# Kernel optimization log

Hardware: AMD Instinct MI355X
Metric: run time of the kernel (lower is better)

## Reference

```python
import jax, jax.numpy as jnp
import numpy as np

N_DRUG = 20000
N_DIS = 20000
D = 128
E = 640000
L = 200000


def _sage(x_src, x_dst, src, dst, Wl, Wr, b, n_dst):
    # SAGEConv: out_i = lin_l(mean_{j in N(i)} x_src_j) + lin_r(x_dst_i)
    msg = x_src[src]                                   # [E, D] gather
    agg = jax.ops.segment_sum(msg, dst, num_segments=n_dst)
    cnt = jax.ops.segment_sum(jnp.ones((src.shape[0],), x_src.dtype), dst,
                              num_segments=n_dst)
    mean = agg / jnp.maximum(cnt, 1.0)[:, None]
    return mean @ Wl + b + x_dst @ Wr


def setup_inputs() -> dict:
    key = jax.random.key(0)
    ks = jax.random.split(key, 24)
    s = 1.0 / np.sqrt(D)
    inp = {
        "x_drug": jax.random.normal(ks[0], (N_DRUG, D), jnp.float32),
        "x_disease": jax.random.normal(ks[1], (N_DIS, D), jnp.float32),
        "ei_d2s": jax.random.randint(ks[2], (2, E), 0, 20000),
        "ei_s2d": jax.random.randint(ks[3], (2, E), 0, 20000),
        "edge_label_index": jax.random.randint(ks[4], (2, L), 0, 20000),
    }
    names = ["W1l_d2s", "W1r_d2s", "W1l_s2d", "W1r_s2d",
             "W2l_d2s", "W2r_d2s", "W2l_s2d", "W2r_s2d"]
    for i, n in enumerate(names):
        inp[n] = jax.random.uniform(ks[5 + i], (D, D), jnp.float32, -s, s)
    for i, n in enumerate(["b1_d2s", "b1_s2d", "b2_d2s", "b2_s2d"]):
        inp[n] = jax.random.uniform(ks[13 + i], (D,), jnp.float32, -s, s)
    inp["dec_W1"] = jax.random.uniform(ks[17], (2 * D, D), jnp.float32, -s, s)
    inp["dec_b1"] = jax.random.uniform(ks[18], (D,), jnp.float32, -s, s)
    inp["dec_W2"] = jax.random.uniform(ks[19], (D, 1), jnp.float32, -s, s)
    inp["dec_b2"] = jax.random.uniform(ks[20], (1,), jnp.float32, -s, s)
    return inp


def reference(x_drug, x_disease,
              W1l_d2s, W1r_d2s, b1_d2s, W1l_s2d, W1r_s2d, b1_s2d,
              W2l_d2s, W2r_d2s, b2_d2s, W2l_s2d, W2r_s2d, b2_s2d,
              dec_W1, dec_b1, dec_W2, dec_b2,
              ei_d2s, ei_s2d, edge_label_index):
    # --- hetero GNN encoder, layer 1 (relu) ---
    h_dis = jax.nn.relu(_sage(x_drug, x_disease, ei_d2s[0], ei_d2s[1],
                              W1l_d2s, W1r_d2s, b1_d2s, N_DIS))
    h_drug = jax.nn.relu(_sage(x_disease, x_drug, ei_s2d[0], ei_s2d[1],
                               W1l_s2d, W1r_s2d, b1_s2d, N_DRUG))
    # --- layer 2 (no activation) ---
    z_dis = _sage(h_drug, h_dis, ei_d2s[0], ei_d2s[1],
                  W2l_d2s, W2r_d2s, b2_d2s, N_DIS)
    z_drug = _sage(h_dis, h_drug, ei_s2d[0], ei_s2d[1],
                   W2l_s2d, W2r_s2d, b2_s2d, N_DRUG)
    # --- edge decoder: gather, concat, 2-layer MLP ---
    row, col = edge_label_index[0], edge_label_index[1]
    z = jnp.concatenate([z_drug[row], z_dis[col]], axis=-1)   # [L, 2D]
    z = jax.nn.relu(z @ dec_W1 + dec_b1)
    z = z @ dec_W2 + dec_b2
    return z.reshape(-1)
```

## Files before the change

### kernel.cpp

```cpp
#include <hip/hip_runtime.h>
#include <hip/hip_fp16.h>

#define D 128
#define NDRUG 20000
#define NDIS 20000
#define EDGES 640000
#define LROWS 200000
#define ROWP 264

typedef unsigned short u16;
typedef __attribute__((ext_vector_type(8))) _Float16 h8v;
typedef __attribute__((ext_vector_type(4))) float f4v;


__device__ inline void h8_load(uint4 u, float f[8]) {
    float2 a = __half22float2(*(const __half2*)&u.x);
    float2 b = __half22float2(*(const __half2*)&u.y);
    float2 c = __half22float2(*(const __half2*)&u.z);
    float2 d = __half22float2(*(const __half2*)&u.w);
    f[0] = a.x; f[1] = a.y; f[2] = b.x; f[3] = b.y;
    f[4] = c.x; f[5] = c.y; f[6] = d.x; f[7] = d.y;
}

__global__ __launch_bounds__(256) void rank2_kernel(
    const int* __restrict__ dA, int* __restrict__ cA, int* __restrict__ rA,
    const int* __restrict__ dB, int* __restrict__ cB, int* __restrict__ rB, int n)
{
    int i = blockIdx.x * blockDim.x + threadIdx.x;
    if (i < n) rA[i] = atomicAdd(&cA[dA[i]], 1);
    else if (i - n < n) rB[i - n] = atomicAdd(&cB[dB[i - n]], 1);
}

__global__ __launch_bounds__(1024) void scan2_kernel(int* __restrict__ c0, int* __restrict__ o0,
                                                     int* __restrict__ c1, int* __restrict__ o1,
                                                     int n) {
    int* cnt_io = (blockIdx.x == 0) ? c0 : c1;
    int* off    = (blockIdx.x == 0) ? o0 : o1;
    __shared__ int wsum[16];
    __shared__ int carry_s;
    const int tid = threadIdx.x;
    const int lane = tid & 63;
    const int wid = tid >> 6;
    if (tid == 0) { carry_s = 0; off[0] = 0; }
    __syncthreads();
    for (int start = 0; start < n; start += 1024) {
        int i = start + tid;
        int v = (i < n) ? cnt_io[i] : 0;
        int carry = carry_s;
        int s = v;
        #pragma unroll
        for (int o = 1; o < 64; o <<= 1) {
            int t = __shfl_up(s, o, 64);
            if (lane >= o) s += t;
        }
        if (lane == 63) wsum[wid] = s;
        __syncthreads();
        if (wid == 0) {
            int ws = (lane < 16) ? wsum[lane] : 0;
            #pragma unroll
            for (int o = 1; o < 16; o <<= 1) {
                int t = __shfl_up(ws, o, 64);
                if (lane >= o) ws += t;
            }
            if (lane < 16) wsum[lane] = ws;
        }
        __syncthreads();
        int woff = (wid > 0) ? wsum[wid - 1] : 0;
        int incl = s + woff + carry;
        if (i < n) {
            off[i + 1] = incl;
            cnt_io[i] = incl - v;
        }
        __syncthreads();
        if (tid == 1023) carry_s = incl;
        __syncthreads();
    }
}

#define SB 104

__global__ __launch_bounds__(256) void scatter_sliced_kernel(
    const int* __restrict__ srcA, const int* __restrict__ dstA,
    const int* __restrict__ rkA, const int* __restrict__ offA, u16* __restrict__ csrA,
    const int* __restrict__ srcB, const int* __restrict__ dstB,
    const int* __restrict__ rkB, const int* __restrict__ offB, u16* __restrict__ csrB,
    int n)
{
    int b = blockIdx.x;
    int dirB = (b >= 8 * SB);
    int bb = b - (dirB ? 8 * SB : 0);
    int s = bb & 7;
    int sub = bb >> 3;
    const int* src = dirB ? srcB : srcA;
    const int* dst = dirB ? dstB : dstA;
    const int* rk  = dirB ? rkB : rkA;
    const int* off = dirB ? offB : offA;
    u16* csr = dirB ? csrB : csrA;

    const int lo = s * 2500, hi = lo + 2500;
    const int chunk = (n + SB - 1) / SB;
    int i0 = sub * chunk;
    int i1 = i0 + chunk; i1 = i1 < n ? i1 : n;
    for (int i = i0 + threadIdx.x; i < i1; i += 256) {
        int d = dst[i];
        if (d >= lo && d < hi) {
            int pos = off[d] + rk[i];
            csr[pos] = (u16)src[i];
        }
    }
}


__global__ __launch_bounds__(256) void cvt16_kernel(const float* __restrict__ in,
                                                    __half* __restrict__ out, int n4) {
    int i = blockIdx.x * blockDim.x + threadIdx.x;
    if (i >= n4) return;
    float4 v = ((const float4*)in)[i];
    __half2 a = __floats2half2_rn(v.x, v.y);
    __half2 b = __floats2half2_rn(v.z, v.w);
    uint2 u;
    u.x = *(unsigned*)&a;
    u.y = *(unsigned*)&b;
    ((uint2*)out)[i] = u;
}

__global__ __launch_bounds__(256) void cvtwt_kernel(
    const float* __restrict__ W1l_d2s, const float* __restrict__ W1r_d2s,
    const float* __restrict__ W1l_s2d, const float* __restrict__ W1r_s2d,
    const float* __restrict__ W2l_d2s, const float* __restrict__ W2r_d2s,
    const float* __restrict__ W2l_s2d, const float* __restrict__ W2r_s2d,
    const float* __restrict__ decW1, __half* __restrict__ out)
{
    int gid = blockIdx.x * 256 + threadIdx.x;
    float v;
    if (gid < 4 * 32768) {
        int chunk = gid >> 15;
        int r = gid & 32767;
        int col = r >> 8;
        int k = r & 255;
        const float *Wl, *Wr;
        switch (chunk) {
            case 0: Wl = W1l_d2s; Wr = W1r_d2s; break;
            case 1: Wl = W1l_s2d; Wr = W1r_s2d; break;
            case 2: Wl = W2l_d2s; Wr = W2r_d2s; break;
            default: Wl = W2l_s2d; Wr = W2r_s2d; break;
        }
        const float* src = (k < 128) ? Wl : Wr;
        v = src[(size_t)(k & 127) * D + col];
    } else {
        int r = gid - 4 * 32768;
        int chunk = r >> 14;
        int q = r & 16383;
        int col = q >> 7;
        int k = q & 127;
        int row = k + (chunk == 0 ? 128 : 0);
        v = decW1[(size_t)row * D + col];
    }
    out[gid] = __float2half_rn(v);
}


__device__ inline void sage_gather(
    const __half* __restrict__ xsrc, const __half* __restrict__ xdst,
    const int* __restrict__ off, const u16* __restrict__ csr,
    __half sm[16][ROWP], int node0, int row0, int lane)
{
    const bool hiHalf = lane >= 32;
    const int lq = lane & 31;
    const int c0 = lq * 4;
    for (int r = 0; r < 4; ++r) {
        int node = node0 + r;
        int e0 = off[node], e1 = off[node + 1];
        int deg = e1 - e0;
        float a0 = 0.f, a1 = 0.f, a2 = 0.f, a3 = 0.f;
        for (int base = e0; base < e1; base += 64) {
            int nv = e1 - base; nv = nv < 64 ? nv : 64;
            int myidx = 0;
            if (lane < nv) myidx = csr[base + lane];
            int npair = nv >> 1;
            int t = 0;
            for (; t + 4 <= npair; t += 4) {
                int pa0 = __builtin_amdgcn_readlane(myidx, 2 * t + 0);
                int pb0 = __builtin_amdgcn_readlane(myidx, 2 * t + 1);
                int pa1 = __builtin_amdgcn_readlane(myidx, 2 * t + 2);
                int pb1 = __builtin_amdgcn_readlane(myidx, 2 * t + 3);
                int pa2 = __builtin_amdgcn_readlane(myidx, 2 * t + 4);
                int pb2 = __builtin_amdgcn_readlane(myidx, 2 * t + 5);
                int pa3 = __builtin_amdgcn_readlane(myidx, 2 * t + 6);
                int pb3 = __builtin_amdgcn_readlane(myidx, 2 * t + 7);
                int s0 = hiHalf ? pb0 : pa0;
                int s1 = hiHalf ? pb1 : pa1;
                int s2 = hiHalf ? pb2 : pa2;
                int s3 = hiHalf ? pb3 : pa3;
                uint2 u0 = *(const uint2*)(xsrc + (size_t)s0 * D + c0);
                uint2 u1 = *(const uint2*)(xsrc + (size_t)s1 * D + c0);
                uint2 u2 = *(const uint2*)(xsrc + (size_t)s2 * D + c0);
                uint2 u3 = *(const uint2*)(xsrc + (size_t)s3 * D + c0);
                float2 t0, t1;
                t0 = __half22float2(*(const __half2*)&u0.x);
                t1 = __half22float2(*(const __half2*)&u0.y);
                a0 += t0.x; a1 += t0.y; a2 += t1.x; a3 += t1.y;
                t0 = __half22float2(*(const __half2*)&u1.x);
                t1 = __half22float2(*(const __half2*)&u1.y);
                a0 += t0.x; a1 += t0.y; a2 += t1.x; a3 += t1.y;
                t0 = __half22float2(*(const __half2*)&u2.x);
                t1 = __half22float2(*(const __half2*)&u2.y);
                a0 += t0.x; a1 += t0.y; a2 += t1.x; a3 += t1.y;
                t0 = __half22float2(*(const __half2*)&u3.x);
                t1 = __half22float2(*(const __half2*)&u3.y);
                a0 += t0.x; a1 += t0.y; a2 += t1.x; a3 += t1.y;
            }
            for (; t < npair; ++t) {
                int pa = __builtin_amdgcn_readlane(myidx, 2 * t + 0);
                int pb = __builtin_amdgcn_readlane(myidx, 2 * t + 1);
                int s = hiHalf ? pb : pa;
                uint2 u = *(const uint2*)(xsrc + (size_t)s * D + c0);
                float2 t0 = __half22float2(*(const __half2*)&u.x);
                float2 t1 = __half22float2(*(const __half2*)&u.y);
                a0 += t0.x; a1 += t0.y; a2 += t1.x; a3 += t1.y;
            }
            if (nv & 1) {
                int s = __builtin_amdgcn_readlane(myidx, nv - 1);
                if (!hiHalf) {
                    uint2 u = *(const uint2*)(xsrc + (size_t)s * D + c0);
                    float2 t0 = __half22float2(*(const __half2*)&u.x);
                    float2 t1 = __half22float2(*(const __half2*)&u.y);
                    a0 += t0.x; a1 += t0.y; a2 += t1.x; a3 += t1.y;
                }
            }
        }
        a0 += __shfl_xor(a0, 32, 64);
        a1 += __shfl_xor(a1, 32, 64);
        a2 += __shfl_xor(a2, 32, 64);
        a3 += __shfl_xor(a3, 32, 64);
        float inv = 1.0f / (float)(deg < 1 ? 1 : deg);
        if (!hiHalf) {
            __half2 h01 = __floats2half2_rn(a0 * inv, a1 * inv);
            __half2 h23 = __floats2half2_rn(a2 * inv, a3 * inv);
            uint2 w; w.x = *(unsigned*)&h01; w.y = *(unsigned*)&h23;
            *(uint2*)&sm[row0 + r][c0] = w;
        } else {
            uint2 u = *(const uint2*)(xdst + (size_t)node * D + c0);
            *(uint2*)&sm[row0 + r][128 + c0] = u;
        }
    }
}


__global__ __launch_bounds__(256, 4) void sage_l1_kernel(
    const __half* __restrict__ xsA, const __half* __restrict__ xdA,
    const int* __restrict__ offA, const u16* __restrict__ csrA,
    const __half* __restrict__ wTA, const float* __restrict__ bA, __half* __restrict__ outA,
    const __half* __restrict__ xsB, const __half* __restrict__ xdB,
    const int* __restrict__ offB, const u16* __restrict__ csrB,
    const __half* __restrict__ wTB, const float* __restrict__ bB, __half* __restrict__ outB)
{
    __shared__ __align__(16) __half sm[16][ROWP];
    const int s8 = blockIdx.x & 7;
    const int bank = s8 >> 2;
    const int blk = ((int)blockIdx.x >> 3) * 4 + (s8 & 3);
    if (blk >= NDIS / 16) return;
    const __half* xsrc = bank ? xsB : xsA;
    const __half* xdst = bank ? xdB : xdA;
    const int* off = bank ? offB : offA;
    const u16* csr = bank ? csrB : csrA;
    const __half* wT = bank ? wTB : wTA;
    const float* bias = bank ? bB : bA;
    __half* out16 = bank ? outB : outA;

    const int lane = threadIdx.x & 63;
    const int wid = threadIdx.x >> 6;
    const int node0 = blk * 16;

    sage_gather(xsrc, xdst, off, csr, sm, node0 + wid * 4, wid * 4, lane);
    __syncthreads();

    const int lr = lane & 15;
    const int g = lane >> 4;
    const int colbase = wid * 32;
    f4v acc0 = {0.f, 0.f, 0.f, 0.f};
    f4v acc1 = {0.f, 0.f, 0.f, 0.f};
    #pragma unroll
    for (int t = 0; t < 8; ++t) {
        h8v a = *(const h8v*)&sm[lr][t * 32 + g * 8];
        h8v b0 = *(const h8v*)(wT + (size_t)(colbase + lr) * 256 + t * 32 + g * 8);
        h8v b1 = *(const h8v*)(wT + (size_t)(colbase + 16 + lr) * 256 + t * 32 + g * 8);
        acc0 = __builtin_amdgcn_mfma_f32_16x16x32_f16(a, b0, acc0, 0, 0, 0);
        acc1 = __builtin_amdgcn_mfma_f32_16x16x32_f16(a, b1, acc1, 0, 0, 0);
    }
    #pragma unroll
    for (int reg = 0; reg < 4; ++reg) {
        int row = g * 4 + reg;
        int col0 = colbase + lr;
        int col1 = colbase + 16 + lr;
        float v0 = fmaxf(acc0[reg] + bias[col0], 0.f);
        float v1 = fmaxf(acc1[reg] + bias[col1], 0.f);
        out16[(size_t)(node0 + row) * D + col0] = __float2half_rn(v0);
        out16[(size_t)(node0 + row) * D + col1] = __float2half_rn(v1);
    }
}

__global__ __launch_bounds__(256, 4) void sage_l2_kernel(
    const __half* __restrict__ xsA, const __half* __restrict__ xdA,
    const int* __restrict__ offA, const u16* __restrict__ csrA,
    const __half* __restrict__ wTA, const float* __restrict__ bA,
    const __half* __restrict__ wdTA, const float* __restrict__ pbA, __half* __restrict__ PoutA,
    const __half* __restrict__ xsB, const __half* __restrict__ xdB,
    const int* __restrict__ offB, const u16* __restrict__ csrB,
    const __half* __restrict__ wTB, const float* __restrict__ bB,
    const __half* __restrict__ wdTB, const float* __restrict__ pbB, __half* __restrict__ PoutB)
{
    __shared__ __align__(16) __half sm[16][ROWP];
    const int s8 = blockIdx.x & 7;
    const int bank = s8 >> 2;
    const int blk = ((int)blockIdx.x >> 3) * 4 + (s8 & 3);
    if (blk >= NDIS / 16) return;
    const __half* xsrc = bank ? xsB : xsA;
    const __half* xdst = bank ? xdB : xdA;
    const int* off = bank ? offB : offA;
    const u16* csr = bank ? csrB : csrA;
    const __half* wT = bank ? wTB : wTA;
    const float* bias = bank ? bB : bA;
    const __half* wdT = bank ? wdTB : wdTA;
    const float* pb = bank ? pbB : pbA;
    __half* Pout = bank ? PoutB : PoutA;

    const int lane = threadIdx.x & 63;
    const int wid = threadIdx.x >> 6;
    const int node0 = blk * 16;

    sage_gather(xsrc, xdst, off, csr, sm, node0 + wid * 4, wid * 4, lane);
    __syncthreads();

    const int lr = lane & 15;
    const int g = lane >> 4;
    const int colbase = wid * 32;
    f4v acc0 = {0.f, 0.f, 0.f, 0.f};
    f4v acc1 = {0.f, 0.f, 0.f, 0.f};
    #pragma unroll
    for (int t = 0; t < 8; ++t) {
        h8v a = *(const h8v*)&sm[lr][t * 32 + g * 8];
        h8v b0 = *(const h8v*)(wT + (size_t)(colbase + lr) * 256 + t * 32 + g * 8);
        h8v b1 = *(const h8v*)(wT + (size_t)(colbase + 16 + lr) * 256 + t * 32 + g * 8);
        acc0 = __builtin_amdgcn_mfma_f32_16x16x32_f16(a, b0, acc0, 0, 0, 0);
        acc1 = __builtin_amdgcn_mfma_f32_16x16x32_f16(a, b1, acc1, 0, 0, 0);
    }

    __syncthreads();
    #pragma unroll
    for (int reg = 0; reg < 4; ++reg) {
        int row = g * 4 + reg;
        sm[row][colbase + lr] = __float2half_rn(acc0[reg] + bias[colbase + lr]);
        sm[row][colbase + 16 + lr] = __float2half_rn(acc1[reg] + bias[colbase + 16 + lr]);
    }
    __syncthreads();

    f4v p0 = {0.f, 0.f, 0.f, 0.f};
    f4v p1 = {0.f, 0.f, 0.f, 0.f};
    #pragma unroll
    for (int t = 0; t < 4; ++t) {
        h8v a = *(const h8v*)&sm[lr][t * 32 + g * 8];
        h8v b0 = *(const h8v*)(wdT + (size_t)(colbase + lr) * 128 + t * 32 + g * 8);
        h8v b1 = *(const h8v*)(wdT + (size_t)(colbase + 16 + lr) * 128 + t * 32 + g * 8);
        p0 = __builtin_amdgcn_mfma_f32_16x16x32_f16(a, b0, p0, 0, 0, 0);
        p1 = __builtin_amdgcn_mfma_f32_16x16x32_f16(a, b1, p1, 0, 0, 0);
    }
    #pragma unroll
    for (int reg = 0; reg < 4; ++reg) {
        int row = g * 4 + reg;
        int col0 = colbase + lr;
        int col1 = colbase + 16 + lr;
        float v0 = p0[reg] + (pb ? pb[col0] : 0.f);
        float v1 = p1[reg] + (pb ? pb[col1] : 0.f);
        Pout[(size_t)(node0 + row) * D + col0] = __float2half_rn(v0);
        Pout[(size_t)(node0 + row) * D + col1] = __float2half_rn(v1);
    }
}


__global__ __launch_bounds__(256) void dec_gather_kernel(
    const __half* __restrict__ Pd, const __half* __restrict__ Ps,
    const int* __restrict__ row_idx, const int* __restrict__ col_idx,
    const float* __restrict__ W2, const float* __restrict__ b2,
    float* __restrict__ out, int nrows)
{
    const int lane = threadIdx.x & 63;
    const int wid = threadIdx.x >> 6;
    const int g = lane >> 4;
    const int lq = lane & 15;
    const int wave_id = blockIdx.x * 4 + wid;
    const int e0 = wave_id * 32;
    if (e0 >= nrows) return;

    const int c0 = lq * 8;
    float w2v[8];
    #pragma unroll
    for (int i = 0; i < 8; ++i) w2v[i] = W2[c0 + i];
    float b2v = b2[0];

    #pragma unroll 2
    for (int it = 0; it < 8; ++it) {
        int ei = it * 4 + g;
        int rr = e0 + ei;
        int ri = row_idx[rr];
        int ci = col_idx[rr];
        uint4 ua = *(const uint4*)(Pd + (size_t)ri * D + c0);
        uint4 ub = *(const uint4*)(Ps + (size_t)ci * D + c0);
        float fa[8], fb[8];
        h8_load(ua, fa);
        h8_load(ub, fb);
        float v = 0.f;
        #pragma unroll
        for (int i = 0; i < 8; ++i)
            v = fmaf(fmaxf(fa[i] + fb[i], 0.f), w2v[i], v);
        v += __shfl_xor(v, 1, 64);
        v += __shfl_xor(v, 2, 64);
        v += __shfl_xor(v, 4, 64);
        v += __shfl_xor(v, 8, 64);
        if (lq == 0) out[rr] = v + b2v;
    }
}


extern "C" void kernel_launch(void* const* d_in, const int* in_sizes, int n_in,
                              void* d_out, int out_size, void* d_ws, size_t ws_size,
                              hipStream_t stream) {
    const float* x_drug = (const float*)d_in[0];
    const float* x_dis  = (const float*)d_in[1];
    const int* ei_d2s = (const int*)d_in[2];
    const int* ei_s2d = (const int*)d_in[3];
    const int* ell    = (const int*)d_in[4];
    const float* W1l_d2s = (const float*)d_in[5];
    const float* W1r_d2s = (const float*)d_in[6];
    const float* W1l_s2d = (const float*)d_in[7];
    const float* W1r_s2d = (const float*)d_in[8];
    const float* W2l_d2s = (const float*)d_in[9];
    const float* W2r_d2s = (const float*)d_in[10];
    const float* W2l_s2d = (const float*)d_in[11];
    const float* W2r_s2d = (const float*)d_in[12];
    const float* b1_d2s = (const float*)d_in[13];
    const float* b1_s2d = (const float*)d_in[14];
    const float* b2_d2s = (const float*)d_in[15];
    const float* b2_s2d = (const float*)d_in[16];
    const float* dec_W1 = (const float*)d_in[17];
    const float* dec_b1 = (const float*)d_in[18];
    const float* dec_W2 = (const float*)d_in[19];
    const float* dec_b2 = (const float*)d_in[20];
    float* out = (float*)d_out;

    char* ws = (char*)d_ws;
    size_t o = 0;
    auto take = [&](size_t bytes) -> char* {
        char* p = ws + o;
        o += (bytes + 255) & ~(size_t)255;
        return p;
    };
    int* off_d2s = (int*)take((NDIS + 1) * sizeof(int));
    int* cnt_d2s = (int*)take(NDIS * sizeof(int));
    u16* csr_d2s = (u16*)take((size_t)EDGES * sizeof(u16));
    int* rk_d2s  = (int*)take((size_t)EDGES * sizeof(int));
    int* off_s2d = (int*)take((NDRUG + 1) * sizeof(int));
    int* cnt_s2d = (int*)take(NDRUG * sizeof(int));
    u16* csr_s2d = (u16*)take((size_t)EDGES * sizeof(u16));
    int* rk_s2d  = (int*)take((size_t)EDGES * sizeof(int));
    __half* x16_drug = (__half*)take((size_t)NDRUG * D * sizeof(__half));
    __half* x16_dis  = (__half*)take((size_t)NDIS * D * sizeof(__half));
    __half* h16_dis  = (__half*)take((size_t)NDIS * D * sizeof(__half));
    __half* h16_drug = (__half*)take((size_t)NDRUG * D * sizeof(__half));
    __half* P16_drug = (__half*)take((size_t)NDRUG * D * sizeof(__half));
    __half* P16_dis  = (__half*)take((size_t)NDIS * D * sizeof(__half));
    __half* w16 = (__half*)take((size_t)163840 * sizeof(__half));

    __half* wT_l1_d2s = w16 + 0 * 32768;
    __half* wT_l1_s2d = w16 + 1 * 32768;
    __half* wT_l2_d2s = w16 + 2 * 32768;
    __half* wT_l2_s2d = w16 + 3 * 32768;
    __half* wdT_hi    = w16 + 4 * 32768;
    __half* wdT_lo    = w16 + 4 * 32768 + 16384;

    hipMemsetAsync(cnt_d2s, 0, NDIS * sizeof(int), stream);
    hipMemsetAsync(cnt_s2d, 0, NDRUG * sizeof(int), stream);

    cvtwt_kernel<<<640, 256, 0, stream>>>(
        W1l_d2s, W1r_d2s, W1l_s2d, W1r_s2d,
        W2l_d2s, W2r_d2s, W2l_s2d, W2r_s2d, dec_W1, w16);

    cvt16_kernel<<<(NDRUG * D / 4 + 255) / 256, 256, 0, stream>>>(x_drug, x16_drug, NDRUG * D / 4);
    cvt16_kernel<<<(NDIS * D / 4 + 255) / 256, 256, 0, stream>>>(x_dis, x16_dis, NDIS * D / 4);

    const int EB2 = (2 * EDGES + 255) / 256;
    rank2_kernel<<<EB2, 256, 0, stream>>>(ei_d2s + EDGES, cnt_d2s, rk_d2s,
                                          ei_s2d + EDGES, cnt_s2d, rk_s2d, EDGES);
    scan2_kernel<<<2, 1024, 0, stream>>>(cnt_d2s, off_d2s, cnt_s2d, off_s2d, NDIS);
    scatter_sliced_kernel<<<2 * 8 * SB, 256, 0, stream>>>(
        ei_d2s, ei_d2s + EDGES, rk_d2s, off_d2s, csr_d2s,
        ei_s2d, ei_s2d + EDGES, rk_s2d, off_s2d, csr_s2d, EDGES);

    const int SGRID = ((2 * (NDIS / 16) + 7) / 8) * 8 + 8;

    sage_l1_kernel<<<SGRID, 256, 0, stream>>>(
        x16_drug, x16_dis, off_d2s, csr_d2s, wT_l1_d2s, b1_d2s, h16_dis,
        x16_dis, x16_drug, off_s2d, csr_s2d, wT_l1_s2d, b1_s2d, h16_drug);

    sage_l2_kernel<<<SGRID, 256, 0, stream>>>(
        h16_drug, h16_dis, off_d2s, csr_d2s, wT_l2_d2s, b2_d2s, wdT_hi, dec_b1, P16_dis,
        h16_dis, h16_drug, off_s2d, csr_s2d, wT_l2_s2d, b2_s2d, wdT_lo, nullptr, P16_drug);

    dec_gather_kernel<<<(LROWS / 32 + 3) / 4, 256, 0, stream>>>(
        P16_drug, P16_dis, ell, ell + LROWS, dec_W2, dec_b2, out, LROWS);
}
```

Measured before the change: 260.5 us.

## Build CSR with sliced histogram and atomic cursor scatter, dropping rank arrays

The per-edge rank kernel, which stored atomicAdd results in rank arrays, is replaced by a destination-sliced histogram that only counts. The scatter then claims CSR slots with atomicAdd on the exclusive-scan cursors that scan2 already leaves in cnt. This removes the rank array writes and reads. The two feature conversion launches are also merged into one kernel. Neighbor order within each CSR row now becomes nondeterministic, which can change fp summation order slightly, and the scatter now does atomics where it used to do plain reads.

```diff
diff --git a/kernel.cpp b/kernel.cpp
--- a/kernel.cpp
+++ b/kernel.cpp
@@ -22,13 +22,30 @@
     f[4] = c.x; f[5] = c.y; f[6] = d.x; f[7] = d.y;
 }
 
-__global__ __launch_bounds__(256) void rank2_kernel(
-    const int* __restrict__ dA, int* __restrict__ cA, int* __restrict__ rA,
-    const int* __restrict__ dB, int* __restrict__ cB, int* __restrict__ rB, int n)
-{
-    int i = blockIdx.x * blockDim.x + threadIdx.x;
-    if (i < n) rA[i] = atomicAdd(&cA[dA[i]], 1);
-    else if (i - n < n) rB[i - n] = atomicAdd(&cB[dB[i - n]], 1);
+
+#define HS 13
+#define SB 104
+
+__global__ __launch_bounds__(256) void hist_sliced_kernel(
+    const int* __restrict__ dstA, int* __restrict__ cntA,
+    const int* __restrict__ dstB, int* __restrict__ cntB, int n)
+{
+    int b = blockIdx.x;
+    int dirB = (b >= 8 * HS);
+    int bb = b - (dirB ? 8 * HS : 0);
+    int s = bb & 7;
+    int sub = bb >> 3;
+    const int* dst = dirB ? dstB : dstA;
+    int* cnt = dirB ? cntB : cntA;
+
+    const int lo = s * 2500, hi = lo + 2500;
+    const int chunk = (n + HS - 1) / HS;
+    int i0 = sub * chunk;
+    int i1 = i0 + chunk; i1 = i1 < n ? i1 : n;
+    for (int i = i0 + threadIdx.x; i < i1; i += 256) {
+        int d = dst[i];
+        if (d >= lo && d < hi) atomicAdd(&cnt[d], 1);
+    }
 }
 
 __global__ __launch_bounds__(1024) void scan2_kernel(int* __restrict__ c0, int* __restrict__ o0,
@@ -77,14 +94,11 @@
     }
 }
 
-#define SB 104
-
-__global__ __launch_bounds__(256) void scatter_sliced_kernel(
+__global__ __launch_bounds__(256) void scatter_atomic_kernel(
     const int* __restrict__ srcA, const int* __restrict__ dstA,
-    const int* __restrict__ rkA, const int* __restrict__ offA, u16* __restrict__ csrA,
+    int* __restrict__ curA, u16* __restrict__ csrA,
     const int* __restrict__ srcB, const int* __restrict__ dstB,
-    const int* __restrict__ rkB, const int* __restrict__ offB, u16* __restrict__ csrB,
-    int n)
+    int* __restrict__ curB, u16* __restrict__ csrB, int n)
 {
     int b = blockIdx.x;
     int dirB = (b >= 8 * SB);
@@ -93,8 +107,7 @@
     int sub = bb >> 3;
     const int* src = dirB ? srcB : srcA;
     const int* dst = dirB ? dstB : dstA;
-    const int* rk  = dirB ? rkB : rkA;
-    const int* off = dirB ? offB : offA;
+    int* cur = dirB ? curB : curA;
     u16* csr = dirB ? csrB : csrA;
 
     const int lo = s * 2500, hi = lo + 2500;
@@ -104,24 +117,29 @@
     for (int i = i0 + threadIdx.x; i < i1; i += 256) {
         int d = dst[i];
         if (d >= lo && d < hi) {
-            int pos = off[d] + rk[i];
+            int pos = atomicAdd(&cur[d], 1);
             csr[pos] = (u16)src[i];
         }
     }
 }
 
 
-__global__ __launch_bounds__(256) void cvt16_kernel(const float* __restrict__ in,
-                                                    __half* __restrict__ out, int n4) {
+__global__ __launch_bounds__(256) void cvt16x2_kernel(
+    const float* __restrict__ ina, __half* __restrict__ outa, int n4a,
+    const float* __restrict__ inb, __half* __restrict__ outb, int n4b)
+{
     int i = blockIdx.x * blockDim.x + threadIdx.x;
-    if (i >= n4) return;
-    float4 v = ((const float4*)in)[i];
+    const float* in; __half* out; int idx;
+    if (i < n4a) { in = ina; out = outa; idx = i; }
+    else if (i - n4a < n4b) { in = inb; out = outb; idx = i - n4a; }
+    else return;
+    float4 v = ((const float4*)in)[idx];
     __half2 a = __floats2half2_rn(v.x, v.y);
     __half2 b = __floats2half2_rn(v.z, v.w);
     uint2 u;
     u.x = *(unsigned*)&a;
     u.y = *(unsigned*)&b;
-    ((uint2*)out)[i] = u;
+    ((uint2*)out)[idx] = u;
 }
 
 __global__ __launch_bounds__(256) void cvtwt_kernel(
@@ -458,11 +476,9 @@
     int* off_d2s = (int*)take((NDIS + 1) * sizeof(int));
     int* cnt_d2s = (int*)take(NDIS * sizeof(int));
     u16* csr_d2s = (u16*)take((size_t)EDGES * sizeof(u16));
-    int* rk_d2s  = (int*)take((size_t)EDGES * sizeof(int));
     int* off_s2d = (int*)take((NDRUG + 1) * sizeof(int));
     int* cnt_s2d = (int*)take(NDRUG * sizeof(int));
     u16* csr_s2d = (u16*)take((size_t)EDGES * sizeof(u16));
-    int* rk_s2d  = (int*)take((size_t)EDGES * sizeof(int));
     __half* x16_drug = (__half*)take((size_t)NDRUG * D * sizeof(__half));
     __half* x16_dis  = (__half*)take((size_t)NDIS * D * sizeof(__half));
     __half* h16_dis  = (__half*)take((size_t)NDIS * D * sizeof(__half));
@@ -485,16 +501,15 @@
         W1l_d2s, W1r_d2s, W1l_s2d, W1r_s2d,
         W2l_d2s, W2r_d2s, W2l_s2d, W2r_s2d, dec_W1, w16);
 
-    cvt16_kernel<<<(NDRUG * D / 4 + 255) / 256, 256, 0, stream>>>(x_drug, x16_drug, NDRUG * D / 4);
-    cvt16_kernel<<<(NDIS * D / 4 + 255) / 256, 256, 0, stream>>>(x_dis, x16_dis, NDIS * D / 4);
-
-    const int EB2 = (2 * EDGES + 255) / 256;
-    rank2_kernel<<<EB2, 256, 0, stream>>>(ei_d2s + EDGES, cnt_d2s, rk_d2s,
-                                          ei_s2d + EDGES, cnt_s2d, rk_s2d, EDGES);
+    cvt16x2_kernel<<<(2 * NDRUG * D / 4 + 255) / 256, 256, 0, stream>>>(
+        x_drug, x16_drug, NDRUG * D / 4, x_dis, x16_dis, NDIS * D / 4);
+
+    hist_sliced_kernel<<<2 * 8 * HS, 256, 0, stream>>>(
+        ei_d2s + EDGES, cnt_d2s, ei_s2d + EDGES, cnt_s2d, EDGES);
     scan2_kernel<<<2, 1024, 0, stream>>>(cnt_d2s, off_d2s, cnt_s2d, off_s2d, NDIS);
-    scatter_sliced_kernel<<<2 * 8 * SB, 256, 0, stream>>>(
-        ei_d2s, ei_d2s + EDGES, rk_d2s, off_d2s, csr_d2s,
-        ei_s2d, ei_s2d + EDGES, rk_s2d, off_s2d, csr_s2d, EDGES);
+    scatter_atomic_kernel<<<2 * 8 * SB, 256, 0, stream>>>(
+        ei_d2s, ei_d2s + EDGES, cnt_d2s, csr_d2s,
+        ei_s2d, ei_s2d + EDGES, cnt_s2d, csr_s2d, EDGES);
 
     const int SGRID = ((2 * (NDIS / 16) + 7) / 8) * 8 + 8;
 
```

Result: slower. 316.8 us (+21.6%).
